# Performance work log

Measured on AMD Instinct MI355X. Metric: run time of the kernel, lower is better.

Reference implementation:

```python
import jax, jax.numpy as jnp
import numpy as np

P1, PW, DIM, DEPTH, HEADS, DH, MAXREL = 4, 256, 1024, 12, 16, 64, 200
INNER = HEADS * DH
MLP = 4 * DIM
NCLS = 40
KSIZE, SIGMA = 20, 2.0


def _gauss_kernel():
    x = np.arange(KSIZE, dtype=np.float32)
    mean = (KSIZE - 1) / 2.0
    k = np.exp(-0.5 * ((x - mean) / SIGMA) ** 2) / (SIGMA * np.sqrt(2.0 * np.pi))
    k = k / k.sum()
    return jnp.asarray(k, jnp.float32)


def _ln(x, g, b, eps=1e-5):
    m = x.mean(-1, keepdims=True)
    v = ((x - m) ** 2).mean(-1, keepdims=True)
    return (x - m) * jax.lax.rsqrt(v + eps) * g + b


def setup_inputs() -> dict:
    key = jax.random.key(0)
    ks = iter(jax.random.split(key, 48))
    def rn(shape, s=0.02):
        return jax.random.normal(next(ks), shape, jnp.float32) * s
    pd = P1 * PW
    return dict(
        neuralInput=jax.random.normal(next(ks), (4, 2048, PW), jnp.float32),
        patch_ln1_g=jnp.ones((pd,), jnp.float32), patch_ln1_b=jnp.zeros((pd,), jnp.float32),
        patch_w=rn((DIM, pd)), patch_b=jnp.zeros((DIM,), jnp.float32),
        patch_ln2_g=jnp.ones((DIM,), jnp.float32), patch_ln2_b=jnp.zeros((DIM,), jnp.float32),
        attn_ln_g=jnp.ones((DEPTH, DIM), jnp.float32), attn_ln_b=jnp.zeros((DEPTH, DIM), jnp.float32),
        qkv_w=rn((DEPTH, 3 * INNER, DIM)),
        out_w=rn((DEPTH, DIM, INNER)), out_b=jnp.zeros((DEPTH, DIM), jnp.float32),
        rel_tab=rn((DEPTH, 2 * MAXREL - 1)),
        ffn_ln_g=jnp.ones((DEPTH, DIM), jnp.float32), ffn_ln_b=jnp.zeros((DEPTH, DIM), jnp.float32),
        ffn_w1=rn((DEPTH, MLP, DIM)), ffn_b1=jnp.zeros((DEPTH, MLP), jnp.float32),
        ffn_w2=rn((DEPTH, DIM, MLP)), ffn_b2=jnp.zeros((DEPTH, DIM), jnp.float32),
        final_ln_g=jnp.ones((DIM,), jnp.float32), final_ln_b=jnp.zeros((DIM,), jnp.float32),
        proj_w=rn((NCLS + 1, DIM)), proj_b=jnp.zeros((NCLS + 1,), jnp.float32),
        X_len=jax.random.randint(jax.random.key(7), (4,), 1, 2048, jnp.int32),
    )


def reference(neuralInput, patch_ln1_g, patch_ln1_b, patch_w, patch_b,
              patch_ln2_g, patch_ln2_b, attn_ln_g, attn_ln_b, qkv_w,
              out_w, out_b, rel_tab, ffn_ln_g, ffn_ln_b, ffn_w1, ffn_b1,
              ffn_w2, ffn_b2, final_ln_g, final_ln_b, proj_w, proj_b, X_len):
    # Gaussian smoothing: depthwise conv1d over time, padding 'same' (k=20 -> pads (9,10))
    xc = jnp.transpose(neuralInput, (0, 2, 1))  # (B, F, T)
    w = jnp.broadcast_to(_gauss_kernel(), (PW, 1, KSIZE))
    xc = jax.lax.conv_general_dilated(xc, w, (1,), [(9, 10)],
                                      dimension_numbers=('NCH', 'OIH', 'NCH'),
                                      feature_group_count=PW)
    x = jnp.transpose(xc, (0, 2, 1))  # (B, T, F)
    B, T, F = x.shape
    N = T // P1
    # patchify: 'b 1 (n p1) (1 p2) -> b n (p1 p2)'
    x = x.reshape(B, N, P1 * PW)
    x = _ln(x, patch_ln1_g, patch_ln1_b)
    x = x @ patch_w.T + patch_b
    x = _ln(x, patch_ln2_g, patch_ln2_b)

    i = jnp.arange(N)[:, None]
    j = jnp.arange(N)[None, :]
    rel = jnp.clip(i - j, -(MAXREL - 1), MAXREL - 1) + MAXREL - 1  # (N, N)
    causal = j <= i  # (N, N)
    scale = DH ** -0.5

    for l in range(DEPTH):
        h = _ln(x, attn_ln_g[l], attn_ln_b[l])
        qkv = h @ qkv_w[l].T  # (B, N, 3*INNER)
        q, k, v = jnp.split(qkv, 3, axis=-1)
        split_heads = lambda t: t.reshape(B, N, HEADS, DH).transpose(0, 2, 1, 3)
        q, k, v = split_heads(q), split_heads(k), split_heads(v)
        dots = jnp.einsum('bhid,bhjd->bhij', q, k) * scale
        dots = dots + rel_tab[l][rel][None, None]  # learned relative-position bias
        dots = jnp.where(causal[None, None], dots, -jnp.inf)
        attn = jax.nn.softmax(dots, axis=-1)
        o = jnp.einsum('bhij,bhjd->bhid', attn, v)
        o = o.transpose(0, 2, 1, 3).reshape(B, N, INNER)
        x = o @ out_w[l].T + out_b[l] + x
        h = _ln(x, ffn_ln_g[l], ffn_ln_b[l])
        h = jax.nn.gelu(h @ ffn_w1[l].T + ffn_b1[l], approximate=False)
        x = h @ ffn_w2[l].T + ffn_b2[l] + x

    x = _ln(x, final_ln_g, final_ln_b)
    return x @ proj_w.T + proj_b  # (B, N, NCLS+1)
```

## Files before the change

kernel.cpp:

```cpp
#include <hip/hip_runtime.h>
#include <math.h>

typedef unsigned short u16;
typedef __attribute__((ext_vector_type(8))) short short8;
typedef __attribute__((ext_vector_type(4))) float f32x4;

static __device__ __forceinline__ u16 f2bf(float f) {
  union { float f; unsigned int u; } v; v.f = f;
  unsigned int u = v.u;
  u = u + 0x7fffu + ((u >> 16) & 1u);
  return (u16)(u >> 16);
}

typedef __attribute__((address_space(3))) void* lds_as_t;
typedef const __attribute__((address_space(1))) void* gbl_as_t;
static __device__ __forceinline__ void gload_lds16(const void* g, void* l) {
  __builtin_amdgcn_global_load_lds((gbl_as_t)g, (lds_as_t)l, 16, 0, 0);
}

static __device__ __forceinline__ void block_reduce2(float& s1, float& s2, float* sh) {
#pragma unroll
  for (int off = 32; off > 0; off >>= 1) {
    s1 += __shfl_xor(s1, off);
    s2 += __shfl_xor(s2, off);
  }
  int tid = threadIdx.x, wv = tid >> 6, lane = tid & 63;
  if (lane == 0) { sh[wv] = s1; sh[4 + wv] = s2; }
  __syncthreads();
  s1 = sh[0] + sh[1] + sh[2] + sh[3];
  s2 = sh[4] + sh[5] + sh[6] + sh[7];
}

__global__ __launch_bounds__(256) void cvt_bf16_k(const float* __restrict__ in,
                                                  u16* __restrict__ out, int n4) {
  int i = blockIdx.x * 256 + threadIdx.x;
  if (i >= n4) return;
  float4 v = ((const float4*)in)[i];
  ushort4 h; h.x = f2bf(v.x); h.y = f2bf(v.y); h.z = f2bf(v.z); h.w = f2bf(v.w);
  ((ushort4*)out)[i] = h;
}
__global__ __launch_bounds__(256) void cvt_pad_k(const float* __restrict__ in,
                                                 u16* __restrict__ out, int n4src, int n4tot) {
  int i = blockIdx.x * 256 + threadIdx.x;
  if (i >= n4tot) return;
  ushort4 h; h.x = 0; h.y = 0; h.z = 0; h.w = 0;
  if (i < n4src) {
    float4 v = ((const float4*)in)[i];
    h.x = f2bf(v.x); h.y = f2bf(v.y); h.z = f2bf(v.z); h.w = f2bf(v.w);
  }
  ((ushort4*)out)[i] = h;
}

__global__ __launch_bounds__(256) void smooth_patch_ln(
    const float* __restrict__ in, const float* __restrict__ g,
    const float* __restrict__ b, u16* __restrict__ out) {
  __shared__ float sh[8];
  int row = blockIdx.x;
  int bb = row >> 9, n = row & 511;
  int f = threadIdx.x;
  float gk[20]; float gs = 0.f;
#pragma unroll
  for (int k = 0; k < 20; ++k) {
    float d = ((float)k - 9.5f) * 0.5f;
    gk[k] = __expf(-0.5f * d * d);
    gs += gk[k];
  }
  float inv = 1.f / gs;
  const float* base = in + (size_t)bb * 2048 * 256 + f;
  float vals[4]; float s1 = 0.f, s2 = 0.f;
#pragma unroll
  for (int tt = 0; tt < 4; ++tt) {
    int t = n * 4 + tt;
    float a = 0.f;
#pragma unroll
    for (int k = 0; k < 20; ++k) {
      int ts = t + k - 9;
      if (ts >= 0 && ts < 2048) a += gk[k] * base[(size_t)ts * 256];
    }
    a *= inv;
    vals[tt] = a; s1 += a; s2 += a * a;
  }
  block_reduce2(s1, s2, sh);
  float mean = s1 * (1.f / 1024.f);
  float var = s2 * (1.f / 1024.f) - mean * mean;
  float rstd = rsqrtf(var + 1e-5f);
#pragma unroll
  for (int tt = 0; tt < 4; ++tt) {
    int idx = tt * 256 + f;
    float o = (vals[tt] - mean) * rstd * g[idx] + b[idx];
    out[(size_t)row * 1024 + idx] = f2bf(o);
  }
}

template <bool OBF16>
__global__ __launch_bounds__(256) void ln_kernel(
    const float* __restrict__ x, const float* __restrict__ g,
    const float* __restrict__ b, void* __restrict__ outp) {
  __shared__ float sh[8];
  int row = blockIdx.x, tid = threadIdx.x;
  float4 v = ((const float4*)(x + (size_t)row * 1024))[tid];
  float s1 = v.x + v.y + v.z + v.w;
  float s2 = v.x * v.x + v.y * v.y + v.z * v.z + v.w * v.w;
  block_reduce2(s1, s2, sh);
  float mean = s1 * (1.f / 1024.f);
  float var = s2 * (1.f / 1024.f) - mean * mean;
  float rstd = rsqrtf(var + 1e-5f);
  float4 gv = ((const float4*)g)[tid];
  float4 bv = ((const float4*)b)[tid];
  float o0 = (v.x - mean) * rstd * gv.x + bv.x;
  float o1 = (v.y - mean) * rstd * gv.y + bv.y;
  float o2 = (v.z - mean) * rstd * gv.z + bv.z;
  float o3 = (v.w - mean) * rstd * gv.w + bv.w;
  if (OBF16) {
    ushort4 h; h.x = f2bf(o0); h.y = f2bf(o1); h.z = f2bf(o2); h.w = f2bf(o3);
    ((ushort4*)outp)[(size_t)row * 256 + tid] = h;
  } else {
    float4 o; o.x = o0; o.y = o1; o.z = o2; o.w = o3;
    ((float4*)outp)[(size_t)row * 256 + tid] = o;
  }
}

template <int EPI, int BM, bool BF16B>
__global__ __launch_bounds__(256) void gemm_kernel(
    const u16* __restrict__ A, const void* __restrict__ Wp,
    const float* __restrict__ bias, const float* __restrict__ res,
    void* __restrict__ outp, int M, int N, int K, int Ksplit) {
  constexpr int MT = BM / 32;
  __shared__ u16 As[BM * 32];
  __shared__ u16 Bs[128 * 32];
  int tid = threadIdx.x;
  int lane = tid & 63, wv = tid >> 6;
  int quad = lane >> 4, l16 = lane & 15;
  int wm = wv >> 1, wn = wv & 1;
  int m0 = blockIdx.x * BM, n0 = blockIdx.y * 128;
  int z = blockIdx.z;
  int kbeg = z * Ksplit, kend = kbeg + Ksplit;
  int sr = lane & 15, sc = lane >> 4;
  const u16* Wb = (const u16*)Wp;
  const float* Wf = (const float*)Wp;
  f32x4 acc[MT][4] = {};

  for (int k0 = kbeg; k0 < kend; k0 += 32) {
    __syncthreads();
#pragma unroll
    for (int i = 0; i < BM / 64; ++i) {
      int g = wv + 4 * i;
      gload_lds16(A + (size_t)(m0 + g * 16 + sr) * K + k0 + sc * 8, &As[g * 512]);
    }
    if constexpr (BF16B) {
#pragma unroll
      for (int i = 0; i < 2; ++i) {
        int g = wv + 4 * i;
        gload_lds16(Wb + (size_t)(n0 + g * 16 + sr) * K + k0 + sc * 8, &Bs[g * 512]);
      }
    } else {
#pragma unroll
      for (int it = 0; it < 2; ++it) {
        int cid = it * 256 + tid;
        int g = cid >> 6, rem = cid & 63, c = rem >> 4, r = rem & 15;
        int gn = n0 + g * 16 + r;
        float4 wa = make_float4(0.f, 0.f, 0.f, 0.f), wb = wa;
        if (gn < N) {
          const float* wp = Wf + (size_t)gn * K + k0 + c * 8;
          wa = *(const float4*)wp; wb = *(const float4*)(wp + 4);
        }
        ushort4 h0, h1;
        h0.x = f2bf(wa.x); h0.y = f2bf(wa.y); h0.z = f2bf(wa.z); h0.w = f2bf(wa.w);
        h1.x = f2bf(wb.x); h1.y = f2bf(wb.y); h1.z = f2bf(wb.z); h1.w = f2bf(wb.w);
        *(ushort4*)&Bs[g * 512 + c * 128 + r * 8] = h0;
        *(ushort4*)&Bs[g * 512 + c * 128 + r * 8 + 4] = h1;
      }
    }
    __syncthreads();
    short8 af[MT], bf[4];
#pragma unroll
    for (int mt = 0; mt < MT; ++mt)
      af[mt] = *(const short8*)&As[(wm * MT + mt) * 512 + quad * 128 + l16 * 8];
#pragma unroll
    for (int nt = 0; nt < 4; ++nt)
      bf[nt] = *(const short8*)&Bs[(wn * 4 + nt) * 512 + quad * 128 + l16 * 8];
#pragma unroll
    for (int mt = 0; mt < MT; ++mt)
#pragma unroll
      for (int nt = 0; nt < 4; ++nt)
        acc[mt][nt] = __builtin_amdgcn_mfma_f32_16x16x32_bf16(af[mt], bf[nt], acc[mt][nt], 0, 0, 0);
  }

  float* outf = (float*)outp;
  u16* outh = (u16*)outp;
  size_t zoff = (size_t)z * M * N;
#pragma unroll
  for (int nt = 0; nt < 4; ++nt) {
    int col = n0 + wn * 64 + nt * 16 + l16;
    if (col >= N) continue;
    float bv = (EPI == 1 || EPI == 4) ? 0.f : bias[col];
#pragma unroll
    for (int mt = 0; mt < MT; ++mt) {
      int rowb = m0 + wm * (BM / 2) + mt * 16 + quad * 4;
#pragma unroll
      for (int r = 0; r < 4; ++r) {
        size_t idx = (size_t)(rowb + r) * N + col;
        float v = acc[mt][nt][r] + bv;
        if (EPI == 0) outf[idx] = v;
        else if (EPI == 1) outh[idx] = f2bf(v);
        else if (EPI == 2) outf[idx] = v + res[idx];
        else if (EPI == 3) outh[idx] = f2bf(0.5f * v * (1.f + erff(v * 0.70710678118f)));
        else outf[zoff + idx] = v;
      }
    }
  }
}

template <bool RES>
__global__ __launch_bounds__(256) void reduce4_k(
    const float* __restrict__ P, const float* __restrict__ bias,
    const float* __restrict__ res, float* __restrict__ out,
    int MN, int NS) {
  int i = blockIdx.x * 256 + threadIdx.x;
  int e = i * 4;
  if (e >= MN) return;
  float4 s = ((const float4*)P)[i];
  for (int z = 1; z < NS; ++z) {
    float4 p = *(const float4*)(P + (size_t)z * MN + e);
    s.x += p.x; s.y += p.y; s.z += p.z; s.w += p.w;
  }
  int col = e & 1023;
  float4 b4 = *(const float4*)(bias + col);
  s.x += b4.x; s.y += b4.y; s.z += b4.z; s.w += b4.w;
  if (RES) {
    float4 r4 = ((const float4*)res)[i];
    s.x += r4.x; s.y += r4.y; s.z += r4.z; s.w += r4.w;
  }
  ((float4*)out)[i] = s;
}

__global__ __launch_bounds__(64) void reduce_proj_k(
    const float* __restrict__ P, const float* __restrict__ bias,
    float* __restrict__ out, int NS) {
  int row = blockIdx.x, col = threadIdx.x;
  if (col >= 41) return;
  float s = 0.f;
  for (int z = 0; z < NS; ++z) s += P[(size_t)z * 2048 * 41 + row * 41 + col];
  out[row * 41 + col] = s + bias[col];
}

__global__ __launch_bounds__(256) void attn_kernel(
    const u16* __restrict__ qkv, const float* __restrict__ rel,
    u16* __restrict__ o) {
  __shared__ u16 Ks[64 * 64];
  __shared__ u16 Vt[64 * 64];
  __shared__ u16 Ps[4][16 * 64];
  __shared__ float rel_s[399];
  int tid = threadIdx.x;
  int qt = blockIdx.x, bh = blockIdx.y;
  int bb = bh >> 4, h = bh & 15;
  for (int i = tid; i < 399; i += 256) rel_s[i] = rel[i];
  int wv = tid >> 6, lane = tid & 63, quad = lane >> 4, l16 = lane & 15;

  int qrow = qt * 64 + wv * 16 + l16;
  const u16* qptr = qkv + ((size_t)(bb * 512 + qrow) * 3072 + h * 64 + quad * 8);
  short8 aq0 = *reinterpret_cast<const short8*>(qptr);
  short8 aq1 = *reinterpret_cast<const short8*>(qptr + 32);

  f32x4 od[4] = {};
  float m_i[4], l_i[4], alpha[4];
#pragma unroll
  for (int r = 0; r < 4; ++r) { m_i[r] = -1e30f; l_i[r] = 0.f; }

  for (int kt = 0; kt <= qt; ++kt) {
    __syncthreads();
#pragma unroll
    for (int i = 0; i < 2; ++i) {
      int ci = tid + i * 256;
      int krow = ci >> 3, ch = ci & 7;
      const u16* kp = qkv + ((size_t)(bb * 512 + kt * 64 + krow) * 3072 + 1024 + h * 64 + ch * 8);
      *reinterpret_cast<uint4*>(&Ks[krow * 64 + ch * 8]) = *reinterpret_cast<const uint4*>(kp);
      u16 vvv[8];
      *reinterpret_cast<uint4*>(vvv) = *reinterpret_cast<const uint4*>(kp + 1024);
#pragma unroll
      for (int jj = 0; jj < 8; ++jj) Vt[(ch * 8 + jj) * 64 + krow] = vvv[jj];
    }
    __syncthreads();
    f32x4 s[4];
#pragma unroll
    for (int nt = 0; nt < 4; ++nt) {
      f32x4 zacc = {};
      short8 b0 = *reinterpret_cast<const short8*>(&Ks[(nt * 16 + l16) * 64 + quad * 8]);
      short8 b1 = *reinterpret_cast<const short8*>(&Ks[(nt * 16 + l16) * 64 + 32 + quad * 8]);
      zacc = __builtin_amdgcn_mfma_f32_16x16x32_bf16(aq0, b0, zacc, 0, 0, 0);
      zacc = __builtin_amdgcn_mfma_f32_16x16x32_bf16(aq1, b1, zacc, 0, 0, 0);
      s[nt] = zacc;
    }
    int ibase = qt * 64 + wv * 16 + quad * 4;
#pragma unroll
    for (int nt = 0; nt < 4; ++nt) {
      int j = kt * 64 + nt * 16 + l16;
#pragma unroll
      for (int r = 0; r < 4; ++r) {
        int d = ibase + r - j;
        float v = s[nt][r] * 0.125f;
        v = (d >= 0) ? v + rel_s[(d > 199 ? 199 : d) + 199] : -1e30f;
        s[nt][r] = v;
      }
    }
#pragma unroll
    for (int r = 0; r < 4; ++r) {
      float mx = fmaxf(fmaxf(s[0][r], s[1][r]), fmaxf(s[2][r], s[3][r]));
#pragma unroll
      for (int off = 1; off < 16; off <<= 1) mx = fmaxf(mx, __shfl_xor(mx, off));
      float mn = fmaxf(m_i[r], mx);
      alpha[r] = __expf(m_i[r] - mn);
      m_i[r] = mn;
      float rs = 0.f;
#pragma unroll
      for (int nt = 0; nt < 4; ++nt) { float p = __expf(s[nt][r] - mn); s[nt][r] = p; rs += p; }
#pragma unroll
      for (int off = 1; off < 16; off <<= 1) rs += __shfl_xor(rs, off);
      l_i[r] = l_i[r] * alpha[r] + rs;
    }
#pragma unroll
    for (int nt = 0; nt < 4; ++nt)
#pragma unroll
      for (int r = 0; r < 4; ++r)
        Ps[wv][(quad * 4 + r) * 64 + nt * 16 + l16] = f2bf(s[nt][r]);
#pragma unroll
    for (int t = 0; t < 4; ++t)
#pragma unroll
      for (int r = 0; r < 4; ++r) od[t][r] *= alpha[r];
    __syncthreads();
#pragma unroll
    for (int t = 0; t < 4; ++t) {
#pragma unroll
      for (int kf = 0; kf < 2; ++kf) {
        short8 pa = *reinterpret_cast<const short8*>(&Ps[wv][l16 * 64 + kf * 32 + quad * 8]);
        short8 vb = *reinterpret_cast<const short8*>(&Vt[(t * 16 + l16) * 64 + kf * 32 + quad * 8]);
        od[t] = __builtin_amdgcn_mfma_f32_16x16x32_bf16(pa, vb, od[t], 0, 0, 0);
      }
    }
  }
#pragma unroll
  for (int t = 0; t < 4; ++t) {
#pragma unroll
    for (int r = 0; r < 4; ++r) {
      int row = qt * 64 + wv * 16 + quad * 4 + r;
      float v = od[t][r] / l_i[r];
      o[(size_t)(bb * 512 + row) * 1024 + h * 64 + t * 16 + l16] = f2bf(v);
    }
  }
}

extern "C" void kernel_launch(void* const* d_in, const int* in_sizes, int n_in,
                              void* d_out, int out_size, void* d_ws, size_t ws_size,
                              hipStream_t stream) {
  const float* neuralInput = (const float*)d_in[0];
  const float* p_ln1_g = (const float*)d_in[1];
  const float* p_ln1_b = (const float*)d_in[2];
  const float* patch_w = (const float*)d_in[3];
  const float* patch_b = (const float*)d_in[4];
  const float* p_ln2_g = (const float*)d_in[5];
  const float* p_ln2_b = (const float*)d_in[6];
  const float* attn_ln_g = (const float*)d_in[7];
  const float* attn_ln_b = (const float*)d_in[8];
  const float* qkv_w = (const float*)d_in[9];
  const float* out_w = (const float*)d_in[10];
  const float* out_b = (const float*)d_in[11];
  const float* rel_tab = (const float*)d_in[12];
  const float* ffn_ln_g = (const float*)d_in[13];
  const float* ffn_ln_b = (const float*)d_in[14];
  const float* ffn_w1 = (const float*)d_in[15];
  const float* ffn_b1 = (const float*)d_in[16];
  const float* ffn_w2 = (const float*)d_in[17];
  const float* ffn_b2 = (const float*)d_in[18];
  const float* fin_g = (const float*)d_in[19];
  const float* fin_b = (const float*)d_in[20];
  const float* proj_w = (const float*)d_in[21];
  const float* proj_b = (const float*)d_in[22];

  char* ws = (char*)d_ws;
  u16* H = (u16*)ws;
  float* X = (float*)(ws + (4ull << 20));
  u16* QKV = (u16*)(ws + (12ull << 20));
  u16* O = (u16*)(ws + (24ull << 20));

  const bool full = ws_size >= 384040960ull;
  dim3 blk(256);

  if (full) {
    u16* G = (u16*)(ws + (28ull << 20));
    float* P = (float*)(ws + (44ull << 20));
    u16* Wb = (u16*)(ws + (76ull << 20));
    u16* qkvB = Wb;
    u16* outB = qkvB + 37748736ull;
    u16* ffn1B = outB + 12582912ull;
    u16* ffn2B = ffn1B + 50331648ull;
    u16* patchB = ffn2B + 50331648ull;
    u16* projB = patchB + 1048576ull;

    cvt_bf16_k<<<(9437184 + 255) / 256, blk, 0, stream>>>(qkv_w, qkvB, 9437184);
    cvt_bf16_k<<<(3145728 + 255) / 256, blk, 0, stream>>>(out_w, outB, 3145728);
    cvt_bf16_k<<<(12582912 + 255) / 256, blk, 0, stream>>>(ffn_w1, ffn1B, 12582912);
    cvt_bf16_k<<<(12582912 + 255) / 256, blk, 0, stream>>>(ffn_w2, ffn2B, 12582912);
    cvt_bf16_k<<<(262144 + 255) / 256, blk, 0, stream>>>(patch_w, patchB, 262144);
    cvt_pad_k<<<(32768 + 255) / 256, blk, 0, stream>>>(proj_w, projB, 10496, 32768);

    smooth_patch_ln<<<2048, blk, 0, stream>>>(neuralInput, p_ln1_g, p_ln1_b, H);
    gemm_kernel<4, 128, true><<<dim3(16, 8, 2), blk, 0, stream>>>(H, patchB, nullptr, nullptr, P, 2048, 1024, 1024, 512);
    reduce4_k<false><<<2048, blk, 0, stream>>>(P, patch_b, nullptr, X, 2097152, 2);
    ln_kernel<false><<<2048, blk, 0, stream>>>(X, p_ln2_g, p_ln2_b, X);

    for (int l = 0; l < 12; ++l) {
      ln_kernel<true><<<2048, blk, 0, stream>>>(X, attn_ln_g + l * 1024, attn_ln_b + l * 1024, H);
      gemm_kernel<1, 128, true><<<dim3(16, 24, 1), blk, 0, stream>>>(H, qkvB + (size_t)l * 3145728, nullptr, nullptr, QKV, 2048, 3072, 1024, 1024);
      attn_kernel<<<dim3(8, 64), blk, 0, stream>>>(QKV, rel_tab + l * 399, O);
      gemm_kernel<4, 128, true><<<dim3(16, 8, 2), blk, 0, stream>>>(O, outB + (size_t)l * 1048576, nullptr, nullptr, P, 2048, 1024, 1024, 512);
      reduce4_k<true><<<2048, blk, 0, stream>>>(P, out_b + l * 1024, X, X, 2097152, 2);
      ln_kernel<true><<<2048, blk, 0, stream>>>(X, ffn_ln_g + l * 1024, ffn_ln_b + l * 1024, H);
      gemm_kernel<3, 128, true><<<dim3(16, 32, 1), blk, 0, stream>>>(H, ffn1B + (size_t)l * 4194304, ffn_b1 + l * 4096, nullptr, G, 2048, 4096, 1024, 1024);
      gemm_kernel<4, 128, true><<<dim3(16, 8, 4), blk, 0, stream>>>(G, ffn2B + (size_t)l * 4194304, nullptr, nullptr, P, 2048, 1024, 4096, 1024);
      reduce4_k<true><<<2048, blk, 0, stream>>>(P, ffn_b2 + l * 1024, X, X, 2097152, 4);
    }

    ln_kernel<true><<<2048, blk, 0, stream>>>(X, fin_g, fin_b, H);
    gemm_kernel<4, 128, true><<<dim3(16, 1, 8), blk, 0, stream>>>(H, projB, nullptr, nullptr, P, 2048, 41, 1024, 128);
    reduce_proj_k<<<2048, 64, 0, stream>>>(P, proj_b, (float*)d_out, 8);
  } else {
    u16* G = (u16*)(ws + (12ull << 20));

    smooth_patch_ln<<<2048, blk, 0, stream>>>(neuralInput, p_ln1_g, p_ln1_b, H);
    gemm_kernel<0, 64, false><<<dim3(32, 8, 1), blk, 0, stream>>>(H, patch_w, patch_b, nullptr, X, 2048, 1024, 1024, 1024);
    ln_kernel<false><<<2048, blk, 0, stream>>>(X, p_ln2_g, p_ln2_b, X);

    for (int l = 0; l < 12; ++l) {
      ln_kernel<true><<<2048, blk, 0, stream>>>(X, attn_ln_g + l * 1024, attn_ln_b + l * 1024, H);
      gemm_kernel<1, 128, false><<<dim3(16, 24, 1), blk, 0, stream>>>(H, qkv_w + (size_t)l * 3145728, nullptr, nullptr, QKV, 2048, 3072, 1024, 1024);
      attn_kernel<<<dim3(8, 64), blk, 0, stream>>>(QKV, rel_tab + l * 399, O);
      gemm_kernel<2, 64, false><<<dim3(32, 8, 1), blk, 0, stream>>>(O, out_w + (size_t)l * 1048576, out_b + l * 1024, X, X, 2048, 1024, 1024, 1024);
      ln_kernel<true><<<2048, blk, 0, stream>>>(X, ffn_ln_g + l * 1024, ffn_ln_b + l * 1024, H);
      gemm_kernel<3, 128, false><<<dim3(16, 32, 1), blk, 0, stream>>>(H, ffn_w1 + (size_t)l * 4194304, ffn_b1 + l * 4096, nullptr, G, 2048, 4096, 1024, 1024);
      gemm_kernel<2, 64, false><<<dim3(32, 8, 1), blk, 0, stream>>>(G, ffn_w2 + (size_t)l * 4194304, ffn_b2 + l * 1024, X, X, 2048, 1024, 4096, 4096);
    }

    ln_kernel<true><<<2048, blk, 0, stream>>>(X, fin_g, fin_b, H);
    gemm_kernel<0, 64, false><<<dim3(32, 1, 1), blk, 0, stream>>>(H, proj_w, proj_b, nullptr, (float*)d_out, 2048, 41, 1024, 1024);
  }
}
```

Measured before the change: 3.158 ms.

## Split-K all GEMMs and fuse residual reduce with following layernorm

Every transformer GEMM now uses split-K (more K slices) writing fp32 partials, followed by reduction kernels. The residual add is fused with the next LayerNorm, and the bias and GELU are fused into the FFN1 reduction. The aim is more parallelism for the small M=2048 GEMMs and fewer separate LN launches. In exchange it adds large fp32 partial-buffer traffic (e.g. 2x 2048x4096 for FFN1) and needs a larger workspace threshold, so the fast path may be skipped if the workspace is smaller.

```diff
diff --git a/kernel.cpp b/kernel.cpp
--- a/kernel.cpp
+++ b/kernel.cpp
@@ -232,6 +232,74 @@
     s.x += r4.x; s.y += r4.y; s.z += r4.z; s.w += r4.w;
   }
   ((float4*)out)[i] = s;
+}
+
+__global__ __launch_bounds__(256) void reduce_bf16_k(
+    const float* __restrict__ P, u16* __restrict__ out, int MN, int NS) {
+  int i = blockIdx.x * 256 + threadIdx.x;
+  int e = i * 4;
+  if (e >= MN) return;
+  float4 s = ((const float4*)P)[i];
+  for (int z = 1; z < NS; ++z) {
+    float4 p = *(const float4*)(P + (size_t)z * MN + e);
+    s.x += p.x; s.y += p.y; s.z += p.z; s.w += p.w;
+  }
+  ushort4 h; h.x = f2bf(s.x); h.y = f2bf(s.y); h.z = f2bf(s.z); h.w = f2bf(s.w);
+  ((ushort4*)out)[i] = h;
+}
+
+__global__ __launch_bounds__(256) void reduce_gelu_k(
+    const float* __restrict__ P, const float* __restrict__ bias,
+    u16* __restrict__ out, int MN, int NS) {
+  int i = blockIdx.x * 256 + threadIdx.x;
+  int e = i * 4;
+  if (e >= MN) return;
+  float4 s = ((const float4*)P)[i];
+  for (int z = 1; z < NS; ++z) {
+    float4 p = *(const float4*)(P + (size_t)z * MN + e);
+    s.x += p.x; s.y += p.y; s.z += p.z; s.w += p.w;
+  }
+  int col = e & 4095;
+  float4 b4 = *(const float4*)(bias + col);
+  s.x += b4.x; s.y += b4.y; s.z += b4.z; s.w += b4.w;
+  ushort4 h;
+  h.x = f2bf(0.5f * s.x * (1.f + erff(s.x * 0.70710678118f)));
+  h.y = f2bf(0.5f * s.y * (1.f + erff(s.y * 0.70710678118f)));
+  h.z = f2bf(0.5f * s.z * (1.f + erff(s.z * 0.70710678118f)));
+  h.w = f2bf(0.5f * s.w * (1.f + erff(s.w * 0.70710678118f)));
+  ((ushort4*)out)[i] = h;
+}
+
+__global__ __launch_bounds__(256) void reduce_ln_k(
+    const float* __restrict__ P, const float* __restrict__ bias,
+    const float* __restrict__ g, const float* __restrict__ b,
+    float* __restrict__ X, u16* __restrict__ H, int NS) {
+  __shared__ float sh[8];
+  int row = blockIdx.x, tid = threadIdx.x;
+  size_t ro = (size_t)row * 256 + tid;
+  float4 s = ((const float4*)P)[ro];
+  for (int z = 1; z < NS; ++z) {
+    float4 p = ((const float4*)(P + (size_t)z * 2097152))[ro];
+    s.x += p.x; s.y += p.y; s.z += p.z; s.w += p.w;
+  }
+  float4 b4 = ((const float4*)bias)[tid];
+  float4 r4 = ((const float4*)X)[ro];
+  s.x += b4.x + r4.x; s.y += b4.y + r4.y; s.z += b4.z + r4.z; s.w += b4.w + r4.w;
+  ((float4*)X)[ro] = s;
+  float s1 = s.x + s.y + s.z + s.w;
+  float s2 = s.x * s.x + s.y * s.y + s.z * s.z + s.w * s.w;
+  block_reduce2(s1, s2, sh);
+  float mean = s1 * (1.f / 1024.f);
+  float var = s2 * (1.f / 1024.f) - mean * mean;
+  float rstd = rsqrtf(var + 1e-5f);
+  float4 gv = ((const float4*)g)[tid];
+  float4 bv = ((const float4*)b)[tid];
+  ushort4 h;
+  h.x = f2bf((s.x - mean) * rstd * gv.x + bv.x);
+  h.y = f2bf((s.y - mean) * rstd * gv.y + bv.y);
+  h.z = f2bf((s.z - mean) * rstd * gv.z + bv.z);
+  h.w = f2bf((s.w - mean) * rstd * gv.w + bv.w);
+  ((ushort4*)H)[ro] = h;
 }
 
 __global__ __launch_bounds__(64) void reduce_proj_k(
@@ -382,13 +450,13 @@
   u16* QKV = (u16*)(ws + (12ull << 20));
   u16* O = (u16*)(ws + (24ull << 20));
 
-  const bool full = ws_size >= 384040960ull;
+  const bool full = ws_size >= 440000000ull;
   dim3 blk(256);
 
   if (full) {
     u16* G = (u16*)(ws + (28ull << 20));
     float* P = (float*)(ws + (44ull << 20));
-    u16* Wb = (u16*)(ws + (76ull << 20));
+    u16* Wb = (u16*)(ws + (108ull << 20));
     u16* qkvB = Wb;
     u16* outB = qkvB + 37748736ull;
     u16* ffn1B = outB + 12582912ull;
@@ -404,23 +472,25 @@
     cvt_pad_k<<<(32768 + 255) / 256, blk, 0, stream>>>(proj_w, projB, 10496, 32768);
 
     smooth_patch_ln<<<2048, blk, 0, stream>>>(neuralInput, p_ln1_g, p_ln1_b, H);
-    gemm_kernel<4, 128, true><<<dim3(16, 8, 2), blk, 0, stream>>>(H, patchB, nullptr, nullptr, P, 2048, 1024, 1024, 512);
-    reduce4_k<false><<<2048, blk, 0, stream>>>(P, patch_b, nullptr, X, 2097152, 2);
+    gemm_kernel<4, 128, true><<<dim3(16, 8, 4), blk, 0, stream>>>(H, patchB, nullptr, nullptr, P, 2048, 1024, 1024, 256);
+    reduce4_k<false><<<2048, blk, 0, stream>>>(P, patch_b, nullptr, X, 2097152, 4);
     ln_kernel<false><<<2048, blk, 0, stream>>>(X, p_ln2_g, p_ln2_b, X);
+    ln_kernel<true><<<2048, blk, 0, stream>>>(X, attn_ln_g, attn_ln_b, H);
 
     for (int l = 0; l < 12; ++l) {
-      ln_kernel<true><<<2048, blk, 0, stream>>>(X, attn_ln_g + l * 1024, attn_ln_b + l * 1024, H);
-      gemm_kernel<1, 128, true><<<dim3(16, 24, 1), blk, 0, stream>>>(H, qkvB + (size_t)l * 3145728, nullptr, nullptr, QKV, 2048, 3072, 1024, 1024);
+      gemm_kernel<4, 128, true><<<dim3(16, 24, 2), blk, 0, stream>>>(H, qkvB + (size_t)l * 3145728, nullptr, nullptr, P, 2048, 3072, 1024, 512);
+      reduce_bf16_k<<<6144, blk, 0, stream>>>(P, QKV, 6291456, 2);
       attn_kernel<<<dim3(8, 64), blk, 0, stream>>>(QKV, rel_tab + l * 399, O);
-      gemm_kernel<4, 128, true><<<dim3(16, 8, 2), blk, 0, stream>>>(O, outB + (size_t)l * 1048576, nullptr, nullptr, P, 2048, 1024, 1024, 512);
-      reduce4_k<true><<<2048, blk, 0, stream>>>(P, out_b + l * 1024, X, X, 2097152, 2);
-      ln_kernel<true><<<2048, blk, 0, stream>>>(X, ffn_ln_g + l * 1024, ffn_ln_b + l * 1024, H);
-      gemm_kernel<3, 128, true><<<dim3(16, 32, 1), blk, 0, stream>>>(H, ffn1B + (size_t)l * 4194304, ffn_b1 + l * 4096, nullptr, G, 2048, 4096, 1024, 1024);
-      gemm_kernel<4, 128, true><<<dim3(16, 8, 4), blk, 0, stream>>>(G, ffn2B + (size_t)l * 4194304, nullptr, nullptr, P, 2048, 1024, 4096, 1024);
-      reduce4_k<true><<<2048, blk, 0, stream>>>(P, ffn_b2 + l * 1024, X, X, 2097152, 4);
-    }
-
-    ln_kernel<true><<<2048, blk, 0, stream>>>(X, fin_g, fin_b, H);
+      gemm_kernel<4, 128, true><<<dim3(16, 8, 4), blk, 0, stream>>>(O, outB + (size_t)l * 1048576, nullptr, nullptr, P, 2048, 1024, 1024, 256);
+      reduce_ln_k<<<2048, blk, 0, stream>>>(P, out_b + l * 1024, ffn_ln_g + l * 1024, ffn_ln_b + l * 1024, X, H, 4);
+      gemm_kernel<4, 128, true><<<dim3(16, 32, 2), blk, 0, stream>>>(H, ffn1B + (size_t)l * 4194304, nullptr, nullptr, P, 2048, 4096, 1024, 512);
+      reduce_gelu_k<<<8192, blk, 0, stream>>>(P, ffn_b1 + l * 4096, G, 8388608, 2);
+      gemm_kernel<4, 128, true><<<dim3(16, 8, 8), blk, 0, stream>>>(G, ffn2B + (size_t)l * 4194304, nullptr, nullptr, P, 2048, 1024, 4096, 512);
+      const float* ng = (l < 11) ? attn_ln_g + (l + 1) * 1024 : fin_g;
+      const float* nb = (l < 11) ? attn_ln_b + (l + 1) * 1024 : fin_b;
+      reduce_ln_k<<<2048, blk, 0, stream>>>(P, ffn_b2 + l * 1024, ng, nb, X, H, 8);
+    }
+
     gemm_kernel<4, 128, true><<<dim3(16, 1, 8), blk, 0, stream>>>(H, projB, nullptr, nullptr, P, 2048, 41, 1024, 128);
     reduce_proj_k<<<2048, 64, 0, stream>>>(P, proj_b, (float*)d_out, 8);
   } else {
```

New measurement: 3.528 ms. 11.7% more time.
